# Kernel optimization log

Measured on AMD Instinct MI355X. Metric: run time of the kernel, lower is better.

## Reference

```python
import jax, jax.numpy as jnp
import numpy as np

B = 524288          # batch of samples
N_LAYERS = 5        # defining_layers
N_WIRES = 4
RING = [(0, 1), (1, 2), (2, 3), (3, 0)]  # qml.broadcast ring pattern


def u3(theta, phi, lam):
    """PennyLane U3 gate. theta/phi/lam may be scalars or [B]; returns [...,2,2] complex64."""
    ct = jnp.cos(theta / 2).astype(jnp.complex64)
    st = jnp.sin(theta / 2).astype(jnp.complex64)
    el = jnp.exp(1j * lam.astype(jnp.complex64))
    ep = jnp.exp(1j * phi.astype(jnp.complex64))
    m00 = ct
    m01 = -el * st
    m10 = ep * st
    m11 = ep * el * ct
    row0 = jnp.stack([m00, m01], axis=-1)
    row1 = jnp.stack([m10, m11], axis=-1)
    return jnp.stack([row0, row1], axis=-2)


def apply_1q(state, gate, wire):
    """state: [B,2,2,2,2]; gate: [2,2] (shared) or [B,2,2] (per-sample)."""
    s = jnp.moveaxis(state, wire + 1, -1)
    if gate.ndim == 3:
        s = jnp.einsum('bij,b...j->b...i', gate, s)
    else:
        s = jnp.einsum('ij,b...j->b...i', gate, s)
    return jnp.moveaxis(s, -1, wire + 1)


def apply_cnot(state, c, t):
    """Flip target axis on the control=1 slice."""
    s = jnp.moveaxis(state, (c + 1, t + 1), (1, 2))  # [B, ctrl, tgt, ...]
    s = jnp.stack([s[:, 0], s[:, 1, ::-1]], axis=1)
    return jnp.moveaxis(s, (1, 2), (c + 1, t + 1))


def setup_inputs() -> dict:
    key = jax.random.key(0)
    kx, kw = jax.random.split(key)
    x = jax.random.normal(kx, (B, N_WIRES), dtype=jnp.float32)
    weights = jax.random.normal(kw, (N_LAYERS, N_WIRES, 3), dtype=jnp.float32)
    return {"x": x, "weights": weights}


def reference(x, weights):
    b = x.shape[0]
    state = jnp.zeros((b, 2, 2, 2, 2), jnp.complex64).at[:, 0, 0, 0, 0].set(1.0)
    # input encoding: U3(x_i, x_i, x_i) on wire i (per-sample gates)
    for i in range(N_WIRES):
        state = apply_1q(state, u3(x[:, i], x[:, i], x[:, i]), i)
    # variational layers: per-wire U3(w0,w1,w2) then ring CNOTs (shared gates)
    for l in range(N_LAYERS):
        for i in range(N_WIRES):
            state = apply_1q(state, u3(weights[l, i, 0], weights[l, i, 1], weights[l, i, 2]), i)
        for c, t in RING:
            state = apply_cnot(state, c, t)
    probs = state.real ** 2 + state.imag ** 2  # [B,2,2,2,2]
    outs = []
    for i in range(N_WIRES):
        p = jnp.moveaxis(probs, i + 1, 1).reshape(b, 2, -1).sum(-1)
        outs.append(p[:, 0] - p[:, 1])  # <Z_i>
    return jnp.stack(outs, axis=-1).astype(jnp.float32)  # [B,4]
```

## Files before the change

### kernel.cpp

```cpp
#include <hip/hip_runtime.h>
#include <math.h>

#define N_LAYERS 5
#define NG 20

__global__ __launch_bounds__(256) void compose_W(const float* __restrict__ w,
                                                 float* __restrict__ W) {
    __shared__ float g[NG][8];
    const int t = threadIdx.x;
    if (t < NG) {
        float th = w[t * 3 + 0], ph = w[t * 3 + 1], la = w[t * 3 + 2];
        float st, ct, sl, cl, sp, cp, spl, cpl;
        sincosf(th * 0.5f, &st, &ct);
        sincosf(la, &sl, &cl);
        sincosf(ph, &sp, &cp);
        sincosf(ph + la, &spl, &cpl);
        g[t][0] = ct;        g[t][1] = 0.0f;
        g[t][2] = -cl * st;  g[t][3] = -sl * st;
        g[t][4] = cp * st;   g[t][5] = sp * st;
        g[t][6] = cpl * ct;  g[t][7] = spl * ct;
    }
    __syncthreads();

    const int row = t & 15;
    const int col = t >> 4;

    float wr = (row == col) ? 1.0f : 0.0f;
    float wi = 0.0f;

#pragma unroll 1
    for (int l = 0; l < N_LAYERS; ++l) {
#pragma unroll
        for (int q = 0; q < 4; ++q) {
            const float* gm = g[l * 4 + q];
            const float m00r = gm[0];
            const float m01r = gm[2], m01i = gm[3];
            const float m10r = gm[4], m10i = gm[5];
            const float m11r = gm[6], m11i = gm[7];
            const int stride = 8 >> q;

            const float pr = __shfl_xor(wr, stride, 64);
            const float pi = __shfl_xor(wi, stride, 64);
            const bool up = (row & stride) != 0;

            const float cAr = up ? m11r : m00r;
            const float cAi = up ? m11i : 0.0f;
            const float cBr = up ? m10r : m01r;
            const float cBi = up ? m10i : m01i;

            const float nr = cAr * wr - cAi * wi + cBr * pr - cBi * pi;
            const float ni = cAr * wi + cAi * wr + cBr * pi + cBi * pr;
            wr = nr; wi = ni;
        }
#pragma unroll
        for (int e = 0; e < 4; ++e) {
            const int cm = 8 >> e;
            const int tm = 8 >> ((e + 1) & 3);
            const float pr = __shfl_xor(wr, tm, 64);
            const float pi = __shfl_xor(wi, tm, 64);
            if (row & cm) { wr = pr; wi = pi; }
        }
    }

    W[(row * 16 + col) * 2 + 0] = wr;
    W[(row * 16 + col) * 2 + 1] = wi;
}

__global__ __launch_bounds__(256) void qmain(const float* __restrict__ x,
                                             const float* __restrict__ W,
                                             float* __restrict__ out) {
    const int b = blockIdx.x * 256 + threadIdx.x;
    const float4 xv = ((const float4*)x)[b];
    const float xs[4] = {xv.x, xv.y, xv.z, xv.w};

    float vr[4][2], vi[4][2];
#pragma unroll
    for (int i = 0; i < 4; i++) {
        const float st = __sinf(xs[i] * 0.5f);
        const float ct = __cosf(xs[i] * 0.5f);
        const float sx = __sinf(xs[i]);
        const float cx = __cosf(xs[i]);
        vr[i][0] = ct;      vi[i][0] = 0.0f;
        vr[i][1] = cx * st; vi[i][1] = sx * st;
    }

    float w01r[4], w01i[4], w23r[4], w23i[4];
#pragma unroll
    for (int a = 0; a < 2; a++) {
#pragma unroll
        for (int c = 0; c < 2; c++) {
            w01r[a * 2 + c] = vr[0][a] * vr[1][c] - vi[0][a] * vi[1][c];
            w01i[a * 2 + c] = vr[0][a] * vi[1][c] + vi[0][a] * vr[1][c];
            w23r[a * 2 + c] = vr[2][a] * vr[3][c] - vi[2][a] * vi[3][c];
            w23i[a * 2 + c] = vr[2][a] * vi[3][c] + vi[2][a] * vr[3][c];
        }
    }
    float sr[16], si[16];
#pragma unroll
    for (int hi = 0; hi < 4; hi++) {
#pragma unroll
        for (int lo = 0; lo < 4; lo++) {
            sr[hi * 4 + lo] = w01r[hi] * w23r[lo] - w01i[hi] * w23i[lo];
            si[hi * 4 + lo] = w01r[hi] * w23i[lo] + w01i[hi] * w23r[lo];
        }
    }

    float p[16];
#pragma unroll
    for (int j = 0; j < 16; j++) {
        float prr = 0.0f, pii = 0.0f;
#pragma unroll
        for (int k = 0; k < 16; k++) {
            const float wr = W[(j * 16 + k) * 2 + 0];
            const float wv = W[(j * 16 + k) * 2 + 1];
            prr = fmaf(wr, sr[k], prr);
            prr = fmaf(-wv, si[k], prr);
            pii = fmaf(wr, si[k], pii);
            pii = fmaf(wv, sr[k], pii);
        }
        p[j] = prr * prr + pii * pii;
    }

    const float a0 = p[0] + p[1],   a1 = p[2] + p[3],   a2 = p[4] + p[5],   a3 = p[6] + p[7];
    const float a4 = p[8] + p[9],   a5 = p[10] + p[11], a6 = p[12] + p[13], a7 = p[14] + p[15];
    const float z3 = (p[0] - p[1]) + (p[2] - p[3]) + (p[4] - p[5]) + (p[6] - p[7])
                   + (p[8] - p[9]) + (p[10] - p[11]) + (p[12] - p[13]) + (p[14] - p[15]);
    const float b0 = a0 + a1, b1 = a2 + a3, b2 = a4 + a5, b3 = a6 + a7;
    const float z2 = (a0 - a1) + (a2 - a3) + (a4 - a5) + (a6 - a7);
    const float c0 = b0 + b1, c1 = b2 + b3;
    const float z1 = (b0 - b1) + (b2 - b3);
    const float z0 = c0 - c1;

    ((float4*)out)[b] = make_float4(z0, z1, z2, z3);
}

extern "C" void kernel_launch(void* const* d_in, const int* in_sizes, int n_in,
                              void* d_out, int out_size, void* d_ws, size_t ws_size,
                              hipStream_t stream) {
    const float* x = (const float*)d_in[0];
    const float* w = (const float*)d_in[1];
    float* out = (float*)d_out;
    float* W = (float*)d_ws;
    const int b = in_sizes[0] / 4;

    compose_W<<<1, 256, 0, stream>>>(w, W);
    qmain<<<b / 256, 256, 0, stream>>>(x, W, out);
}
```

Measured before the change: 75.66 us.

## Fuse unitary composition into main kernel with per-block LDS copy of W

Merges the one-block compose kernel into the batch kernel, so every block recomputes the 16x16 composed unitary in shared memory, and one launch plus the global workspace round trip go away. The matrix-vector loop now reads W from LDS as float4 and accumulates the Z expectations on the fly in a non-unrolled j loop, instead of unrolling 512 scalar global loads. The cost is redundant per-block composition work (sincos, shuffles, two barriers) repeated across about 2048 blocks.

```diff
diff --git a/kernel.cpp b/kernel.cpp
--- a/kernel.cpp
+++ b/kernel.cpp
@@ -4,10 +4,13 @@
 #define N_LAYERS 5
 #define NG 20
 
-__global__ __launch_bounds__(256) void compose_W(const float* __restrict__ w,
-                                                 float* __restrict__ W) {
+__global__ __launch_bounds__(256) void qfused(const float* __restrict__ x,
+                                              const float* __restrict__ w,
+                                              float* __restrict__ out) {
     __shared__ float g[NG][8];
+    __shared__ __align__(16) float Wl[512];
     const int t = threadIdx.x;
+
     if (t < NG) {
         float th = w[t * 3 + 0], ph = w[t * 3 + 1], la = w[t * 3 + 2];
         float st, ct, sl, cl, sp, cp, spl, cpl;
@@ -22,54 +25,51 @@
     }
     __syncthreads();
 
-    const int row = t & 15;
-    const int col = t >> 4;
-
-    float wr = (row == col) ? 1.0f : 0.0f;
-    float wi = 0.0f;
+    {
+        const int row = t & 15;
+        const int col = t >> 4;
+        float wr = (row == col) ? 1.0f : 0.0f;
+        float wi = 0.0f;
 
 #pragma unroll 1
-    for (int l = 0; l < N_LAYERS; ++l) {
+        for (int l = 0; l < N_LAYERS; ++l) {
 #pragma unroll
-        for (int q = 0; q < 4; ++q) {
-            const float* gm = g[l * 4 + q];
-            const float m00r = gm[0];
-            const float m01r = gm[2], m01i = gm[3];
-            const float m10r = gm[4], m10i = gm[5];
-            const float m11r = gm[6], m11i = gm[7];
-            const int stride = 8 >> q;
+            for (int q = 0; q < 4; ++q) {
+                const float* gm = g[l * 4 + q];
+                const float m00r = gm[0];
+                const float m01r = gm[2], m01i = gm[3];
+                const float m10r = gm[4], m10i = gm[5];
+                const float m11r = gm[6], m11i = gm[7];
+                const int stride = 8 >> q;
 
-            const float pr = __shfl_xor(wr, stride, 64);
-            const float pi = __shfl_xor(wi, stride, 64);
-            const bool up = (row & stride) != 0;
+                const float pr = __shfl_xor(wr, stride, 64);
+                const float pi = __shfl_xor(wi, stride, 64);
+                const bool up = (row & stride) != 0;
 
-            const float cAr = up ? m11r : m00r;
-            const float cAi = up ? m11i : 0.0f;
-            const float cBr = up ? m10r : m01r;
-            const float cBi = up ? m10i : m01i;
+                const float cAr = up ? m11r : m00r;
+                const float cAi = up ? m11i : 0.0f;
+                const float cBr = up ? m10r : m01r;
+                const float cBi = up ? m10i : m01i;
 
-            const float nr = cAr * wr - cAi * wi + cBr * pr - cBi * pi;
-            const float ni = cAr * wi + cAi * wr + cBr * pi + cBi * pr;
-            wr = nr; wi = ni;
+                const float nr = cAr * wr - cAi * wi + cBr * pr - cBi * pi;
+                const float ni = cAr * wi + cAi * wr + cBr * pi + cBi * pr;
+                wr = nr; wi = ni;
+            }
+#pragma unroll
+            for (int e = 0; e < 4; ++e) {
+                const int cm = 8 >> e;
+                const int tm = 8 >> ((e + 1) & 3);
+                const float pr = __shfl_xor(wr, tm, 64);
+                const float pi = __shfl_xor(wi, tm, 64);
+                if (row & cm) { wr = pr; wi = pi; }
+            }
         }
-#pragma unroll
-        for (int e = 0; e < 4; ++e) {
-            const int cm = 8 >> e;
-            const int tm = 8 >> ((e + 1) & 3);
-            const float pr = __shfl_xor(wr, tm, 64);
-            const float pi = __shfl_xor(wi, tm, 64);
-            if (row & cm) { wr = pr; wi = pi; }
-        }
+        Wl[(row * 16 + col) * 2 + 0] = wr;
+        Wl[(row * 16 + col) * 2 + 1] = wi;
     }
+    __syncthreads();
 
-    W[(row * 16 + col) * 2 + 0] = wr;
-    W[(row * 16 + col) * 2 + 1] = wi;
-}
-
-__global__ __launch_bounds__(256) void qmain(const float* __restrict__ x,
-                                             const float* __restrict__ W,
-                                             float* __restrict__ out) {
-    const int b = blockIdx.x * 256 + threadIdx.x;
+    const int b = blockIdx.x * 256 + t;
     const float4 xv = ((const float4*)x)[b];
     const float xs[4] = {xv.x, xv.y, xv.z, xv.w};
 
@@ -105,31 +105,34 @@
         }
     }
 
-    float p[16];
-#pragma unroll
-    for (int j = 0; j < 16; j++) {
+    float z0 = 0.0f, z1 = 0.0f, z2 = 0.0f, z3 = 0.0f;
+    const float4* Wv = (const float4*)Wl;
+#pragma unroll 1
+    for (int j = 0; j < 16; ++j) {
         float prr = 0.0f, pii = 0.0f;
 #pragma unroll
-        for (int k = 0; k < 16; k++) {
-            const float wr = W[(j * 16 + k) * 2 + 0];
-            const float wv = W[(j * 16 + k) * 2 + 1];
-            prr = fmaf(wr, sr[k], prr);
-            prr = fmaf(-wv, si[k], prr);
-            pii = fmaf(wr, si[k], pii);
-            pii = fmaf(wv, sr[k], pii);
+        for (int kq = 0; kq < 8; ++kq) {
+            const float4 wv = Wv[j * 8 + kq];
+            const int k0 = kq * 2;
+            prr = fmaf(wv.x, sr[k0], prr);
+            prr = fmaf(-wv.y, si[k0], prr);
+            pii = fmaf(wv.x, si[k0], pii);
+            pii = fmaf(wv.y, sr[k0], pii);
+            prr = fmaf(wv.z, sr[k0 + 1], prr);
+            prr = fmaf(-wv.w, si[k0 + 1], prr);
+            pii = fmaf(wv.z, si[k0 + 1], pii);
+            pii = fmaf(wv.w, sr[k0 + 1], pii);
         }
-        p[j] = prr * prr + pii * pii;
+        const float pj = prr * prr + pii * pii;
+        const float s3 = (j & 1) ? -1.0f : 1.0f;
+        const float s2 = (j & 2) ? -1.0f : 1.0f;
+        const float s1 = (j & 4) ? -1.0f : 1.0f;
+        const float s0 = (j & 8) ? -1.0f : 1.0f;
+        z3 = fmaf(s3, pj, z3);
+        z2 = fmaf(s2, pj, z2);
+        z1 = fmaf(s1, pj, z1);
+        z0 = fmaf(s0, pj, z0);
     }
-
-    const float a0 = p[0] + p[1],   a1 = p[2] + p[3],   a2 = p[4] + p[5],   a3 = p[6] + p[7];
-    const float a4 = p[8] + p[9],   a5 = p[10] + p[11], a6 = p[12] + p[13], a7 = p[14] + p[15];
-    const float z3 = (p[0] - p[1]) + (p[2] - p[3]) + (p[4] - p[5]) + (p[6] - p[7])
-                   + (p[8] - p[9]) + (p[10] - p[11]) + (p[12] - p[13]) + (p[14] - p[15]);
-    const float b0 = a0 + a1, b1 = a2 + a3, b2 = a4 + a5, b3 = a6 + a7;
-    const float z2 = (a0 - a1) + (a2 - a3) + (a4 - a5) + (a6 - a7);
-    const float c0 = b0 + b1, c1 = b2 + b3;
-    const float z1 = (b0 - b1) + (b2 - b3);
-    const float z0 = c0 - c1;
 
     ((float4*)out)[b] = make_float4(z0, z1, z2, z3);
 }
@@ -140,9 +143,7 @@
     const float* x = (const float*)d_in[0];
     const float* w = (const float*)d_in[1];
     float* out = (float*)d_out;
-    float* W = (float*)d_ws;
     const int b = in_sizes[0] / 4;
 
-    compose_W<<<1, 256, 0, stream>>>(w, W);
-    qmain<<<b / 256, 256, 0, stream>>>(x, W, out);
+    qfused<<<b / 256, 256, 0, stream>>>(x, w, out);
 }
```

New measurement: 84.46 us. 1.12x slower.
